# Optimization experiments

Hardware: AMD Instinct MI355X
Metric: run time of the kernel (lower is better)

The kernel has to match this reference:

```python
import jax, jax.numpy as jnp
import numpy as np

GAMMA = 0.99
RHO_THRESHOLD = 1.0
C_THRESHOLD = 1.0
BASELINE_LOSS_SCALING = 0.5
ENT_COEFF = 0.01
PPO_CLIP = 0.2


def setup_inputs() -> dict:
    key = jax.random.key(0)
    ks = jax.random.split(key, 7)
    T, B, A = 512, 8192, 2
    return {
        "prob": jax.random.uniform(ks[0], (T, B, A), dtype=jnp.float32),
        "action_prob": jax.random.uniform(ks[1], (T, B, A), dtype=jnp.float32),
        "v": jax.random.normal(ks[2], (T, B), dtype=jnp.float32),
        "next_v": jax.random.normal(ks[3], (T, B), dtype=jnp.float32),
        "reward": jax.random.normal(ks[4], (T, B), dtype=jnp.float32),
        "action": jax.random.randint(ks[5], (T, B), 0, 2, dtype=jnp.int32),
        "done": jax.random.randint(ks[6], (T, B), 0, 2, dtype=jnp.int32),
    }


def _log_prob(p, a):
    # torch.distributions.Categorical normalizes unnormalized probs
    logp = jnp.log(p) - jnp.log(p.sum(-1, keepdims=True))  # [T,B,A]
    return jnp.take_along_axis(logp, a[..., None].astype(jnp.int32), axis=-1)[..., 0]


def reference(prob, action_prob, v, next_v, reward, action, done):
    done_f = done.astype(v.dtype)  # [T,B]
    logp = _log_prob(prob, action)
    logp_act = _log_prob(action_prob, action)
    ratio = jnp.exp(logp - logp_act)  # [T,B]

    clipped_rho = jnp.minimum(ratio, RHO_THRESHOLD)
    clipped_c = jnp.minimum(ratio, C_THRESHOLD)
    deltas = clipped_rho * (reward + (1.0 - done_f) * GAMMA * next_v - v)

    # V-trace backward recurrence over time (dim 0), vectorized over batch
    def step(next_vtrace, xs):
        v_t, d_t, c_t, rho_t, r_t, nv_t, dn_t = xs
        vt = v_t + d_t + GAMMA * c_t * (next_vtrace - nv_t) * (1.0 - dn_t)
        adv = rho_t * (r_t + GAMMA * next_vtrace * (1.0 - dn_t) - v_t)
        return vt, (vt, adv)

    _, (vtrace, adv) = jax.lax.scan(
        step, next_v[-1],
        (v, deltas, clipped_c, clipped_rho, reward, next_v, done_f),
        reverse=True)

    vtrace = jax.lax.stop_gradient(vtrace)  # .detach() in original
    adv = jax.lax.stop_gradient(adv)

    critic_loss = BASELINE_LOSS_SCALING * jnp.mean((v - vtrace) ** 2)
    surr1 = ratio * adv
    surr2 = jnp.clip(ratio, 1.0 - PPO_CLIP, 1.0 + PPO_CLIP) * adv
    actor_loss = -jnp.minimum(surr1, surr2).mean()

    # entropy is logged but NOT included in total_loss in the original
    total_loss = actor_loss + critic_loss
    return total_loss
```

## Files before the change

kernel.cpp:

```cpp
#include <hip/hip_runtime.h>

#define T_DIM 512
#define B_DIM 8192
#define GB 16
#define NC 64
#define LC 8
#define GAMMA 0.99f

__launch_bounds__(1024, 8)
__global__ void vtrace_main(const float* __restrict__ prob,
                            const float* __restrict__ aprob,
                            const float* __restrict__ v,
                            const float* __restrict__ nv,
                            const float* __restrict__ rw,
                            const int* __restrict__ act,
                            const int* __restrict__ dnn,
                            float* __restrict__ partials) {
    __shared__ float Sc[NC][GB];
    __shared__ float Mc[NC][GB];
    __shared__ float Cin[NC][GB];
    __shared__ float red[32];

    const int tid = threadIdx.x;
    const int bl  = tid & (GB - 1);
    const int c   = tid >> 4;
    const int b   = blockIdx.x * GB + bl;
    const int t0  = c * LC;

    float rs[LC], pp[LC], vv[LC];
    float S = 0.0f, M = 1.0f;

    const float2* __restrict__ prob2  = (const float2*)prob;
    const float2* __restrict__ aprob2 = (const float2*)aprob;

#pragma unroll
    for (int i = LC - 1; i >= 0; --i) {
        const size_t idx = (size_t)(t0 + i) * B_DIM + b;
        float2 pr = prob2[idx];
        float2 qr = aprob2[idx];
        float vvi = v[idx];
        float rr  = rw[idx];
        int   a   = act[idx];
        int   d   = dnn[idx];

        float pa    = a ? pr.y : pr.x;
        float qa    = a ? qr.y : qr.x;
        float ratio = (pa * (qr.x + qr.y)) / ((pr.x + pr.y) * qa);
        float rho   = fminf(ratio, 1.0f);
        float m     = d ? 0.0f : GAMMA * rho;
        float p     = rho * (rr - vvi);

        rs[i] = __uint_as_float(__float_as_uint(ratio) | ((unsigned)d << 31));
        pp[i] = p;
        vv[i] = vvi;
        S = (vvi + p) + m * S;
        M = m * M;
    }

    Sc[c][bl] = S;
    Mc[c][bl] = M;
    __syncthreads();

    if (tid < GB) {
        float carry = nv[(size_t)(T_DIM - 1) * B_DIM + blockIdx.x * GB + tid];
#pragma unroll 8
        for (int cc = NC - 1; cc >= 0; --cc) {
            Cin[cc][tid] = carry;
            carry = fmaf(Mc[cc][tid], carry, Sc[cc][tid]);
        }
    }
    __syncthreads();

    float carry  = Cin[c][bl];
    float critic = 0.0f, msum = 0.0f;
#pragma unroll
    for (int i = LC - 1; i >= 0; --i) {
        const unsigned u = __float_as_uint(rs[i]);
        const float r   = __uint_as_float(u & 0x7fffffffu);
        const float m   = ((int)u < 0) ? 0.0f : GAMMA * fminf(r, 1.0f);
        const float adv = pp[i] + m * carry;
        carry = vv[i] + adv;
        critic = fmaf(adv, adv, critic);
        const float lo = fminf(r, 1.2f);
        const float hi = fmaxf(r, 0.8f);
        msum += (adv >= 0.0f) ? lo * adv : hi * adv;
    }

#pragma unroll
    for (int off = 32; off > 0; off >>= 1) {
        critic += __shfl_down(critic, off, 64);
        msum   += __shfl_down(msum, off, 64);
    }
    const int wave = tid >> 6;
    if ((tid & 63) == 0) { red[wave] = critic; red[16 + wave] = msum; }
    __syncthreads();
    if (tid == 0) {
        float cs = 0.0f, ms = 0.0f;
#pragma unroll
        for (int w = 0; w < 16; ++w) { cs += red[w]; ms += red[16 + w]; }
        partials[blockIdx.x]       = cs;
        partials[512 + blockIdx.x] = ms;
    }
}

__global__ void vtrace_final(const float* __restrict__ partials,
                             float* __restrict__ out) {
    __shared__ float red[16];
    const int tid = threadIdx.x;
    float cs = partials[tid];
    float ms = partials[512 + tid];
#pragma unroll
    for (int off = 32; off > 0; off >>= 1) {
        cs += __shfl_down(cs, off, 64);
        ms += __shfl_down(ms, off, 64);
    }
    const int wave = tid >> 6;
    if ((tid & 63) == 0) { red[wave] = cs; red[8 + wave] = ms; }
    __syncthreads();
    if (tid == 0) {
        float c = 0.0f, m = 0.0f;
#pragma unroll
        for (int w = 0; w < 8; ++w) { c += red[w]; m += red[8 + w]; }
        const float invN = 1.0f / (float)((size_t)T_DIM * B_DIM);
        out[0] = 0.5f * c * invN - m * invN;
    }
}

extern "C" void kernel_launch(void* const* d_in, const int* in_sizes, int n_in,
                              void* d_out, int out_size, void* d_ws, size_t ws_size,
                              hipStream_t stream) {
    const float* prob  = (const float*)d_in[0];
    const float* aprob = (const float*)d_in[1];
    const float* v     = (const float*)d_in[2];
    const float* nv    = (const float*)d_in[3];
    const float* rw    = (const float*)d_in[4];
    const int*   act   = (const int*)d_in[5];
    const int*   dnn   = (const int*)d_in[6];
    float* partials = (float*)d_ws;
    float* out      = (float*)d_out;

    vtrace_main<<<B_DIM / GB, GB * NC, 0, stream>>>(prob, aprob, v, nv, rw,
                                                    act, dnn, partials);
    vtrace_final<<<1, 512, 0, stream>>>(partials, out);
}
```

Baseline: 170.2 us.

## Stream inputs via global_load_lds double-buffering and re-read v/reward in second pass

Restructures the V-trace kernel to use 32 batch columns by 32 chunks of 16 timesteps. Per-timestep inputs are loaded straight into LDS with global_load_lds into a double buffer, with manual waitcnt pipelining. Only the packed ratio/done word is kept in LDS. The second pass reloads v and reward from global memory instead of holding them in registers. This removes the register pressure of the old per-thread arrays, but adds extra global traffic for v and reward, and LDS use grows to about 130KB per block, which limits occupancy.

```diff
diff --git a/kernel.cpp b/kernel.cpp
--- a/kernel.cpp
+++ b/kernel.cpp
@@ -2,88 +2,138 @@
 
 #define T_DIM 512
 #define B_DIM 8192
-#define GB 16
-#define NC 64
-#define LC 8
+#define GBB 32
+#define NCB 32
+#define LCB 16
+#define NTH (GBB * NCB)
 #define GAMMA 0.99f
 
-__launch_bounds__(1024, 8)
-__global__ void vtrace_main(const float* __restrict__ prob,
-                            const float* __restrict__ aprob,
-                            const float* __restrict__ v,
-                            const float* __restrict__ nv,
-                            const float* __restrict__ rw,
-                            const int* __restrict__ act,
-                            const int* __restrict__ dnn,
-                            float* __restrict__ partials) {
-    __shared__ float Sc[NC][GB];
-    __shared__ float Mc[NC][GB];
-    __shared__ float Cin[NC][GB];
+#define GLD(g, l) __builtin_amdgcn_global_load_lds(                          \
+    (const __attribute__((address_space(1))) void*)(g),                      \
+    (__attribute__((address_space(3))) void*)(l), 4, 0, 0)
+
+__global__ __launch_bounds__(NTH)
+void vtrace_main(const float* __restrict__ prob,
+                 const float* __restrict__ aprob,
+                 const float* __restrict__ v,
+                 const float* __restrict__ nv,
+                 const float* __restrict__ rw,
+                 const int* __restrict__ act,
+                 const int* __restrict__ dnn,
+                 float* __restrict__ partials) {
+    __shared__ unsigned int sl[2][8][NTH];
+    __shared__ unsigned int st_r[LCB * NTH];
+    __shared__ float Sc[NTH];
+    __shared__ float Mc[NTH];
+    __shared__ float Cin[NTH];
     __shared__ float red[32];
 
     const int tid = threadIdx.x;
-    const int bl  = tid & (GB - 1);
-    const int c   = tid >> 4;
-    const int b   = blockIdx.x * GB + bl;
-    const int t0  = c * LC;
+    const int bl  = tid & (GBB - 1);
+    const int c   = tid >> 5;
+    const int wb  = tid & ~63;
+    const int b   = blockIdx.x * GBB + bl;
+    const size_t base = (size_t)(c * LCB) * B_DIM + b;
 
-    float rs[LC], pp[LC], vv[LC];
+    const char* prob8  = (const char*)prob;
+    const char* aprob8 = (const char*)aprob;
+    const char* v4     = (const char*)v;
+    const char* rw4    = (const char*)rw;
+    const char* act4   = (const char*)act;
+    const char* dnn4   = (const char*)dnn;
+
+#define STAGE_A(i, k) do {                                                   \
+        const size_t o = base + (size_t)(i) * B_DIM;                         \
+        GLD(prob8  + o * 8,     &sl[k][0][wb]);                              \
+        GLD(prob8  + o * 8 + 4, &sl[k][1][wb]);                              \
+        GLD(aprob8 + o * 8,     &sl[k][2][wb]);                              \
+        GLD(aprob8 + o * 8 + 4, &sl[k][3][wb]);                              \
+        GLD(v4   + o * 4, &sl[k][4][wb]);                                    \
+        GLD(rw4  + o * 4, &sl[k][5][wb]);                                    \
+        GLD(act4 + o * 4, &sl[k][6][wb]);                                    \
+        GLD(dnn4 + o * 4, &sl[k][7][wb]);                                    \
+    } while (0)
+
+#define STAGE_B(i, k) do {                                                   \
+        const size_t o = base + (size_t)(i) * B_DIM;                         \
+        GLD(v4  + o * 4, &sl[k][0][wb]);                                     \
+        GLD(rw4 + o * 4, &sl[k][1][wb]);                                     \
+    } while (0)
+
+    STAGE_A(LCB - 1, 0);
+    STAGE_A(LCB - 2, 1);
+
     float S = 0.0f, M = 1.0f;
+#pragma unroll
+    for (int i = LCB - 1; i >= 0; --i) {
+        const int k = (LCB - 1 - i) & 1;
+        if (i > 0) asm volatile("s_waitcnt vmcnt(8)" ::: "memory");
+        else       asm volatile("s_waitcnt vmcnt(0)" ::: "memory");
 
-    const float2* __restrict__ prob2  = (const float2*)prob;
-    const float2* __restrict__ aprob2 = (const float2*)aprob;
+        const float pxv = __uint_as_float(sl[k][0][tid]);
+        const float pyv = __uint_as_float(sl[k][1][tid]);
+        const float qxv = __uint_as_float(sl[k][2][tid]);
+        const float qyv = __uint_as_float(sl[k][3][tid]);
+        const float vvv = __uint_as_float(sl[k][4][tid]);
+        const float rrv = __uint_as_float(sl[k][5][tid]);
+        const unsigned int aau = sl[k][6][tid];
+        const unsigned int ddu = sl[k][7][tid];
 
-#pragma unroll
-    for (int i = LC - 1; i >= 0; --i) {
-        const size_t idx = (size_t)(t0 + i) * B_DIM + b;
-        float2 pr = prob2[idx];
-        float2 qr = aprob2[idx];
-        float vvi = v[idx];
-        float rr  = rw[idx];
-        int   a   = act[idx];
-        int   d   = dnn[idx];
+        const float pa    = aau ? pyv : pxv;
+        const float qa    = aau ? qyv : qxv;
+        const float ratio = (pa * (qxv + qyv)) / ((pxv + pyv) * qa);
+        const float rho   = fminf(ratio, 1.0f);
+        const float m     = ddu ? 0.0f : GAMMA * rho;
+        const float p     = rho * (rrv - vvv);
 
-        float pa    = a ? pr.y : pr.x;
-        float qa    = a ? qr.y : qr.x;
-        float ratio = (pa * (qr.x + qr.y)) / ((pr.x + pr.y) * qa);
-        float rho   = fminf(ratio, 1.0f);
-        float m     = d ? 0.0f : GAMMA * rho;
-        float p     = rho * (rr - vvi);
+        st_r[i * NTH + tid] = __float_as_uint(ratio) | (ddu << 31);
+        S = (vvv + p) + m * S;
+        M = m * M;
 
-        rs[i] = __uint_as_float(__float_as_uint(ratio) | ((unsigned)d << 31));
-        pp[i] = p;
-        vv[i] = vvi;
-        S = (vvi + p) + m * S;
-        M = m * M;
+        asm volatile("s_waitcnt lgkmcnt(0)" ::: "memory");
+        if (i >= 2) STAGE_A(i - 2, k);
     }
 
-    Sc[c][bl] = S;
-    Mc[c][bl] = M;
+    Sc[tid] = S;
+    Mc[tid] = M;
+
+    STAGE_B(LCB - 1, 0);
+    STAGE_B(LCB - 2, 1);
     __syncthreads();
 
-    if (tid < GB) {
-        float carry = nv[(size_t)(T_DIM - 1) * B_DIM + blockIdx.x * GB + tid];
+    if (tid < GBB) {
+        float carry = nv[(size_t)(T_DIM - 1) * B_DIM + blockIdx.x * GBB + tid];
 #pragma unroll 8
-        for (int cc = NC - 1; cc >= 0; --cc) {
-            Cin[cc][tid] = carry;
-            carry = fmaf(Mc[cc][tid], carry, Sc[cc][tid]);
+        for (int cc = NCB - 1; cc >= 0; --cc) {
+            Cin[cc * GBB + tid] = carry;
+            carry = fmaf(Mc[cc * GBB + tid], carry, Sc[cc * GBB + tid]);
         }
     }
     __syncthreads();
 
-    float carry  = Cin[c][bl];
+    float carry  = Cin[tid];
     float critic = 0.0f, msum = 0.0f;
 #pragma unroll
-    for (int i = LC - 1; i >= 0; --i) {
-        const unsigned u = __float_as_uint(rs[i]);
-        const float r   = __uint_as_float(u & 0x7fffffffu);
-        const float m   = ((int)u < 0) ? 0.0f : GAMMA * fminf(r, 1.0f);
-        const float adv = pp[i] + m * carry;
-        carry = vv[i] + adv;
+    for (int i = LCB - 1; i >= 0; --i) {
+        const int k = (LCB - 1 - i) & 1;
+        if (i > 0) asm volatile("s_waitcnt vmcnt(2)" ::: "memory");
+        else       asm volatile("s_waitcnt vmcnt(0)" ::: "memory");
+
+        const float vvv = __uint_as_float(sl[k][0][tid]);
+        const float rrv = __uint_as_float(sl[k][1][tid]);
+        const unsigned int u = st_r[i * NTH + tid];
+        const float r_  = __uint_as_float(u & 0x7fffffffu);
+        const float m   = ((int)u < 0) ? 0.0f : GAMMA * fminf(r_, 1.0f);
+        const float p   = fminf(r_, 1.0f) * (rrv - vvv);
+        const float t_  = m * carry;
+        const float adv = p + t_;
+        carry = (vvv + p) + t_;
         critic = fmaf(adv, adv, critic);
-        const float lo = fminf(r, 1.2f);
-        const float hi = fmaxf(r, 0.8f);
-        msum += (adv >= 0.0f) ? lo * adv : hi * adv;
+        msum += (adv >= 0.0f) ? fminf(r_, 1.2f) * adv
+                              : fmaxf(r_, 0.8f) * adv;
+
+        asm volatile("s_waitcnt lgkmcnt(0)" ::: "memory");
+        if (i >= 2) STAGE_B(i - 2, k);
     }
 
 #pragma unroll
@@ -99,28 +149,30 @@
 #pragma unroll
         for (int w = 0; w < 16; ++w) { cs += red[w]; ms += red[16 + w]; }
         partials[blockIdx.x]       = cs;
-        partials[512 + blockIdx.x] = ms;
+        partials[256 + blockIdx.x] = ms;
     }
+#undef STAGE_A
+#undef STAGE_B
 }
 
 __global__ void vtrace_final(const float* __restrict__ partials,
                              float* __restrict__ out) {
-    __shared__ float red[16];
+    __shared__ float red[8];
     const int tid = threadIdx.x;
     float cs = partials[tid];
-    float ms = partials[512 + tid];
+    float ms = partials[256 + tid];
 #pragma unroll
     for (int off = 32; off > 0; off >>= 1) {
         cs += __shfl_down(cs, off, 64);
         ms += __shfl_down(ms, off, 64);
     }
     const int wave = tid >> 6;
-    if ((tid & 63) == 0) { red[wave] = cs; red[8 + wave] = ms; }
+    if ((tid & 63) == 0) { red[wave] = cs; red[4 + wave] = ms; }
     __syncthreads();
     if (tid == 0) {
         float c = 0.0f, m = 0.0f;
 #pragma unroll
-        for (int w = 0; w < 8; ++w) { c += red[w]; m += red[8 + w]; }
+        for (int w = 0; w < 4; ++w) { c += red[w]; m += red[4 + w]; }
         const float invN = 1.0f / (float)((size_t)T_DIM * B_DIM);
         out[0] = 0.5f * c * invN - m * invN;
     }
@@ -139,7 +191,7 @@
     float* partials = (float*)d_ws;
     float* out      = (float*)d_out;
 
-    vtrace_main<<<B_DIM / GB, GB * NC, 0, stream>>>(prob, aprob, v, nv, rw,
-                                                    act, dnn, partials);
-    vtrace_final<<<1, 512, 0, stream>>>(partials, out);
+    vtrace_main<<<B_DIM / GBB, NTH, 0, stream>>>(prob, aprob, v, nv, rw,
+                                                 act, dnn, partials);
+    vtrace_final<<<1, 256, 0, stream>>>(partials, out);
 }
```

After: 175.0 us. 1.03x slower.

## Process two batch columns per thread with wider vector loads and LDS staging

Applied to the files above, without the earlier changes.

Each thread now handles two adjacent batch columns, using float4/float2/int2 vector loads so a block covers 32 columns instead of 16. Ratios with packed done bits are staged in shared memory rather than registers, and v and reward are reloaded from global memory in the second pass instead of being kept in registers. This widens memory transactions and halves the grid, at the cost of 64KB+ of LDS per block, which limits occupancy, and extra global rereads of v and reward.

```diff
diff --git a/kernel.cpp b/kernel.cpp
--- a/kernel.cpp
+++ b/kernel.cpp
@@ -2,88 +2,121 @@
 
 #define T_DIM 512
 #define B_DIM 8192
-#define GB 16
-#define NC 64
-#define LC 8
+#define GBB 32
+#define LANES 16
+#define NCB 64
+#define LCB 8
+#define NTH 1024
 #define GAMMA 0.99f
 
-__launch_bounds__(1024, 8)
-__global__ void vtrace_main(const float* __restrict__ prob,
-                            const float* __restrict__ aprob,
-                            const float* __restrict__ v,
-                            const float* __restrict__ nv,
-                            const float* __restrict__ rw,
-                            const int* __restrict__ act,
-                            const int* __restrict__ dnn,
-                            float* __restrict__ partials) {
-    __shared__ float Sc[NC][GB];
-    __shared__ float Mc[NC][GB];
-    __shared__ float Cin[NC][GB];
+__global__ __launch_bounds__(NTH)
+void vtrace_main(const float* __restrict__ prob,
+                 const float* __restrict__ aprob,
+                 const float* __restrict__ v,
+                 const float* __restrict__ nv,
+                 const float* __restrict__ rw,
+                 const int* __restrict__ act,
+                 const int* __restrict__ dnn,
+                 float* __restrict__ partials) {
+    __shared__ unsigned int st_r[T_DIM * GBB];
+    __shared__ float Sc[NCB * GBB];
+    __shared__ float Mc[NCB * GBB];
+    __shared__ float Cin[NCB * GBB];
     __shared__ float red[32];
 
-    const int tid = threadIdx.x;
-    const int bl  = tid & (GB - 1);
-    const int c   = tid >> 4;
-    const int b   = blockIdx.x * GB + bl;
-    const int t0  = c * LC;
+    const int tid  = threadIdx.x;
+    const int l    = tid & (LANES - 1);
+    const int c    = tid >> 4;
+    const int col0 = 2 * l;
 
-    float rs[LC], pp[LC], vv[LC];
-    float S = 0.0f, M = 1.0f;
+    const size_t pbase = (size_t)blockIdx.x * (GBB / 2) + l;
+    const size_t cbase = (size_t)(c * LCB) * (B_DIM / 2) + pbase;
 
-    const float2* __restrict__ prob2  = (const float2*)prob;
-    const float2* __restrict__ aprob2 = (const float2*)aprob;
+    const float4* __restrict__ prob4  = (const float4*)prob;
+    const float4* __restrict__ aprob4 = (const float4*)aprob;
+    const float2* __restrict__ v2     = (const float2*)v;
+    const float2* __restrict__ rw2    = (const float2*)rw;
+    const int2*   __restrict__ act2   = (const int2*)act;
+    const int2*   __restrict__ dnn2   = (const int2*)dnn;
 
+    float S0 = 0.0f, M0 = 1.0f, S1 = 0.0f, M1 = 1.0f;
 #pragma unroll
-    for (int i = LC - 1; i >= 0; --i) {
-        const size_t idx = (size_t)(t0 + i) * B_DIM + b;
-        float2 pr = prob2[idx];
-        float2 qr = aprob2[idx];
-        float vvi = v[idx];
-        float rr  = rw[idx];
-        int   a   = act[idx];
-        int   d   = dnn[idx];
+    for (int i = LCB - 1; i >= 0; --i) {
+        const size_t o = cbase + (size_t)i * (B_DIM / 2);
+        const float4 P = prob4[o];
+        const float4 Q = aprob4[o];
+        const float2 V = v2[o];
+        const float2 R = rw2[o];
+        const int2   A = act2[o];
+        const int2   D = dnn2[o];
 
-        float pa    = a ? pr.y : pr.x;
-        float qa    = a ? qr.y : qr.x;
-        float ratio = (pa * (qr.x + qr.y)) / ((pr.x + pr.y) * qa);
-        float rho   = fminf(ratio, 1.0f);
-        float m     = d ? 0.0f : GAMMA * rho;
-        float p     = rho * (rr - vvi);
+        const float pa0 = A.x ? P.y : P.x;
+        const float qa0 = A.x ? Q.y : Q.x;
+        const float ra0 = (pa0 * (Q.x + Q.y)) / ((P.x + P.y) * qa0);
+        const float rh0 = fminf(ra0, 1.0f);
+        const float m0  = D.x ? 0.0f : GAMMA * rh0;
+        const float p0  = rh0 * (R.x - V.x);
+        const float pa1 = A.y ? P.w : P.z;
+        const float qa1 = A.y ? Q.w : Q.z;
+        const float ra1 = (pa1 * (Q.z + Q.w)) / ((P.z + P.w) * qa1);
+        const float rh1 = fminf(ra1, 1.0f);
+        const float m1  = D.y ? 0.0f : GAMMA * rh1;
+        const float p1  = rh1 * (R.y - V.y);
 
-        rs[i] = __uint_as_float(__float_as_uint(ratio) | ((unsigned)d << 31));
-        pp[i] = p;
-        vv[i] = vvi;
-        S = (vvi + p) + m * S;
-        M = m * M;
+        uint2 st;
+        st.x = __float_as_uint(ra0) | ((unsigned)D.x << 31);
+        st.y = __float_as_uint(ra1) | ((unsigned)D.y << 31);
+        *(uint2*)&st_r[(c * LCB + i) * GBB + col0] = st;
+
+        S0 = (V.x + p0) + m0 * S0;  M0 = m0 * M0;
+        S1 = (V.y + p1) + m1 * S1;  M1 = m1 * M1;
     }
-
-    Sc[c][bl] = S;
-    Mc[c][bl] = M;
+    *(float2*)&Sc[c * GBB + col0] = make_float2(S0, S1);
+    *(float2*)&Mc[c * GBB + col0] = make_float2(M0, M1);
     __syncthreads();
 
-    if (tid < GB) {
-        float carry = nv[(size_t)(T_DIM - 1) * B_DIM + blockIdx.x * GB + tid];
+    if (tid < GBB) {
+        float carry = nv[(size_t)(T_DIM - 1) * B_DIM + blockIdx.x * GBB + tid];
 #pragma unroll 8
-        for (int cc = NC - 1; cc >= 0; --cc) {
-            Cin[cc][tid] = carry;
-            carry = fmaf(Mc[cc][tid], carry, Sc[cc][tid]);
+        for (int cc = NCB - 1; cc >= 0; --cc) {
+            Cin[cc * GBB + tid] = carry;
+            carry = fmaf(Mc[cc * GBB + tid], carry, Sc[cc * GBB + tid]);
         }
     }
     __syncthreads();
 
-    float carry  = Cin[c][bl];
+    const float2 cr = *(const float2*)&Cin[c * GBB + col0];
+    float carry0 = cr.x, carry1 = cr.y;
     float critic = 0.0f, msum = 0.0f;
 #pragma unroll
-    for (int i = LC - 1; i >= 0; --i) {
-        const unsigned u = __float_as_uint(rs[i]);
-        const float r   = __uint_as_float(u & 0x7fffffffu);
-        const float m   = ((int)u < 0) ? 0.0f : GAMMA * fminf(r, 1.0f);
-        const float adv = pp[i] + m * carry;
-        carry = vv[i] + adv;
-        critic = fmaf(adv, adv, critic);
-        const float lo = fminf(r, 1.2f);
-        const float hi = fmaxf(r, 0.8f);
-        msum += (adv >= 0.0f) ? lo * adv : hi * adv;
+    for (int i = LCB - 1; i >= 0; --i) {
+        const size_t o = cbase + (size_t)i * (B_DIM / 2);
+        const float2 V = v2[o];
+        const float2 R = rw2[o];
+        const uint2  u = *(const uint2*)&st_r[(c * LCB + i) * GBB + col0];
+
+        {
+            const float r_  = __uint_as_float(u.x & 0x7fffffffu);
+            const float m   = ((int)u.x < 0) ? 0.0f : GAMMA * fminf(r_, 1.0f);
+            const float p   = fminf(r_, 1.0f) * (R.x - V.x);
+            const float t_  = m * carry0;
+            const float adv = p + t_;
+            carry0 = (V.x + p) + t_;
+            critic = fmaf(adv, adv, critic);
+            msum += (adv >= 0.0f) ? fminf(r_, 1.2f) * adv
+                                  : fmaxf(r_, 0.8f) * adv;
+        }
+        {
+            const float r_  = __uint_as_float(u.y & 0x7fffffffu);
+            const float m   = ((int)u.y < 0) ? 0.0f : GAMMA * fminf(r_, 1.0f);
+            const float p   = fminf(r_, 1.0f) * (R.y - V.y);
+            const float t_  = m * carry1;
+            const float adv = p + t_;
+            carry1 = (V.y + p) + t_;
+            critic = fmaf(adv, adv, critic);
+            msum += (adv >= 0.0f) ? fminf(r_, 1.2f) * adv
+                                  : fmaxf(r_, 0.8f) * adv;
+        }
     }
 
 #pragma unroll
@@ -99,28 +132,28 @@
 #pragma unroll
         for (int w = 0; w < 16; ++w) { cs += red[w]; ms += red[16 + w]; }
         partials[blockIdx.x]       = cs;
-        partials[512 + blockIdx.x] = ms;
+        partials[256 + blockIdx.x] = ms;
     }
 }
 
 __global__ void vtrace_final(const float* __restrict__ partials,
                              float* __restrict__ out) {
-    __shared__ float red[16];
+    __shared__ float red[8];
     const int tid = threadIdx.x;
     float cs = partials[tid];
-    float ms = partials[512 + tid];
+    float ms = partials[256 + tid];
 #pragma unroll
     for (int off = 32; off > 0; off >>= 1) {
         cs += __shfl_down(cs, off, 64);
         ms += __shfl_down(ms, off, 64);
     }
     const int wave = tid >> 6;
-    if ((tid & 63) == 0) { red[wave] = cs; red[8 + wave] = ms; }
+    if ((tid & 63) == 0) { red[wave] = cs; red[4 + wave] = ms; }
     __syncthreads();
     if (tid == 0) {
         float c = 0.0f, m = 0.0f;
 #pragma unroll
-        for (int w = 0; w < 8; ++w) { c += red[w]; m += red[8 + w]; }
+        for (int w = 0; w < 4; ++w) { c += red[w]; m += red[4 + w]; }
         const float invN = 1.0f / (float)((size_t)T_DIM * B_DIM);
         out[0] = 0.5f * c * invN - m * invN;
     }
@@ -139,7 +172,7 @@
     float* partials = (float*)d_ws;
     float* out      = (float*)d_out;
 
-    vtrace_main<<<B_DIM / GB, GB * NC, 0, stream>>>(prob, aprob, v, nv, rw,
-                                                    act, dnn, partials);
-    vtrace_final<<<1, 512, 0, stream>>>(partials, out);
+    vtrace_main<<<B_DIM / GBB, NTH, 0, stream>>>(prob, aprob, v, nv, rw,
+                                                 act, dnn, partials);
+    vtrace_final<<<1, 256, 0, stream>>>(partials, out);
 }
```

After: 174.6 us. 1.03x slower.
